# Kernel optimization log

Measured on AMD Instinct MI355X. Metric: run time of the kernel, lower is better.

The kernel has to match this reference:

```python
import jax, jax.numpy as jnp
import numpy as np

DIM = 512

def setup_inputs() -> dict:
    key = jax.random.key(0)
    ks = jax.random.split(key, 8)
    B, T, S, D = 4, 128, 512, DIM
    scale = 1.0 / np.sqrt(D)
    return {
        "inp": jax.random.normal(ks[0], (B, T, D), jnp.float32),
        "context": jax.random.normal(ks[1], (B, S, D), jnp.float32),
        # linear_query: Linear(D, D, bias=True)
        "Wq": jax.random.normal(ks[2], (D, D), jnp.float32) * scale,
        "bq": jax.random.normal(ks[3], (D,), jnp.float32) * scale,
        # linear_context: Linear(D, D, bias=False)
        "Wc": jax.random.normal(ks[4], (D, D), jnp.float32) * scale,
        # v: Linear(D, 1, bias=False)
        "v": jax.random.normal(ks[5], (D,), jnp.float32) * scale,
        # linear_out: Linear(2D, D, bias=True)
        "Wout": jax.random.normal(ks[6], (D, 2 * D), jnp.float32) * scale,
        "bout": jax.random.normal(ks[7], (D,), jnp.float32) * scale,
    }

def reference(inp, context, Wq, bq, Wc, v, Wout, bout):
    # inp: (B,T,D) target queries; context: (B,S,D) source states
    wq = jnp.einsum('btd,ed->bte', inp, Wq) + bq          # (B,T,D)
    uh = jnp.einsum('bsd,ed->bse', context, Wc)            # (B,S,D)
    # additive (Bahdanau) score: v^T tanh(Wq q_t + Wc h_s)
    wquh = jnp.tanh(wq[:, :, None, :] + uh[:, None, :, :])  # (B,T,S,D)
    align = jnp.einsum('btsd,d->bts', wquh, v)             # (B,T,S)
    align_vectors = jax.nn.softmax(align, axis=-1)          # softmax over src_len
    c = jnp.einsum('bts,bsd->btd', align_vectors, context)  # context vector
    concat_c = jnp.concatenate([c, inp], axis=-1)           # (B,T,2D)
    attn_h = jnp.einsum('btf,ef->bte', concat_c, Wout) + bout  # (B,T,D)
    return attn_h, align_vectors
```

## Files before the change

### kernel.cpp

```cpp
#include <hip/hip_runtime.h>
#include <hip/hip_bf16.h>
#include <math.h>


typedef __attribute__((ext_vector_type(8))) short short8;
typedef __attribute__((ext_vector_type(4))) float f32x4;
typedef unsigned short ushort_t;

static __device__ __forceinline__ unsigned short f2bf(float x) {
    union { __hip_bfloat16 h; unsigned short u; } c;
    c.h = __float2bfloat16(x);
    return c.u;
}
static __device__ __forceinline__ int bf2x(float lo, float hi) {
    return (int)(((unsigned)f2bf(hi) << 16) | (unsigned)f2bf(lo));
}

template<bool BF>
static __device__ __forceinline__ void load16(const void* base, size_t elemoff,
                                              int4& r0, int4& r1) {
    if (BF) {
        const int4* p = (const int4*)((const ushort_t*)base + elemoff);
        r0 = p[0]; r1 = p[1];
    } else {
        const float4* p = (const float4*)((const float*)base + elemoff);
        float4 a = p[0], b = p[1], c = p[2], d = p[3];
        r0.x = bf2x(a.x, a.y); r0.y = bf2x(a.z, a.w);
        r0.z = bf2x(b.x, b.y); r0.w = bf2x(b.z, b.w);
        r1.x = bf2x(c.x, c.y); r1.y = bf2x(c.z, c.w);
        r1.z = bf2x(d.x, d.y); r1.w = bf2x(d.z, d.w);
    }
}

template<bool A_BF, bool W_BF, int EPI>
static __device__ __forceinline__ void gemm_body(
    ushort_t* As, ushort_t* Ws,
    const void* A, const void* W, const float* bias, const float* partial,
    void* Cv, int K, int lda, int ldw, int ldc, int bm, int bn)
{
    const int tid = threadIdx.x;
    const int wave = tid >> 6, lane = tid & 63;
    const int mh = (wave & 1) * 32, nh = (wave >> 1) * 32;
    const int quad = lane >> 4, l16 = lane & 15;
    const int srow = tid >> 2, schunk = tid & 3;

    const size_t aoff = (size_t)(bm + srow) * lda + schunk * 16;
    const size_t woff = (size_t)(bn + srow) * ldw + schunk * 16;
    int4* AsW = (int4*)&As[srow * 72 + schunk * 16];
    int4* WsW = (int4*)&Ws[srow * 72 + schunk * 16];

    f32x4 acc00 = {0.f, 0.f, 0.f, 0.f}, acc01 = acc00, acc10 = acc00, acc11 = acc00;

    int4 a0r, a1r, w0r, w1r;
    load16<A_BF>(A, aoff, a0r, a1r);
    load16<W_BF>(W, woff, w0r, w1r);

    for (int k0 = 0; k0 < K; k0 += 64) {
        AsW[0] = a0r; AsW[1] = a1r;
        WsW[0] = w0r; WsW[1] = w1r;
        __syncthreads();
        if (k0 + 64 < K) {
            load16<A_BF>(A, aoff + k0 + 64, a0r, a1r);
            load16<W_BF>(W, woff + k0 + 64, w0r, w1r);
        }
        #pragma unroll
        for (int kk = 0; kk < 64; kk += 32) {
            short8 a0 = *(const short8*)&As[(mh + l16) * 72 + kk + quad * 8];
            short8 a1 = *(const short8*)&As[(mh + 16 + l16) * 72 + kk + quad * 8];
            short8 b0 = *(const short8*)&Ws[(nh + l16) * 72 + kk + quad * 8];
            short8 b1 = *(const short8*)&Ws[(nh + 16 + l16) * 72 + kk + quad * 8];
            acc00 = __builtin_amdgcn_mfma_f32_16x16x32_bf16(a0, b0, acc00, 0, 0, 0);
            acc01 = __builtin_amdgcn_mfma_f32_16x16x32_bf16(a0, b1, acc01, 0, 0, 0);
            acc10 = __builtin_amdgcn_mfma_f32_16x16x32_bf16(a1, b0, acc10, 0, 0, 0);
            acc11 = __builtin_amdgcn_mfma_f32_16x16x32_bf16(a1, b1, acc11, 0, 0, 0);
        }
        __syncthreads();
    }

    const int col0 = bn + nh + l16;
    const int col1 = col0 + 16;
    float bias0 = bias ? bias[col0] : 0.f;
    float bias1 = bias ? bias[col1] : 0.f;

    f32x4 accs[2][2] = {{acc00, acc01}, {acc10, acc11}};
    #pragma unroll
    for (int mt = 0; mt < 2; ++mt) {
        #pragma unroll
        for (int r = 0; r < 4; ++r) {
            int row = bm + mh + mt * 16 + quad * 4 + r;
            size_t rowoff = (size_t)row * ldc;
            float v0 = accs[mt][0][r] + bias0;
            float v1 = accs[mt][1][r] + bias1;
            if (EPI == 1) { v0 = __expf(2.f * v0); v1 = __expf(2.f * v1); }
            if (EPI == 3) { v0 += partial[rowoff + col0]; v1 += partial[rowoff + col1]; }
            if (EPI == 2) {
                ushort_t* C = (ushort_t*)Cv;
                C[rowoff + col0] = f2bf(v0);
                C[rowoff + col1] = f2bf(v1);
            } else {
                float* C = (float*)Cv;
                C[rowoff + col0] = v0;
                C[rowoff + col1] = v1;
            }
        }
    }
}

__global__ __launch_bounds__(256) void cvt_bf16(
    const float* __restrict__ inp, const float* __restrict__ ctx,
    const float* __restrict__ Wq, const float* __restrict__ Wc,
    const float* __restrict__ Wout,
    ushort_t* __restrict__ inpb, ushort_t* __restrict__ ctxb,
    ushort_t* __restrict__ Wqb, ushort_t* __restrict__ Wcb,
    ushort_t* __restrict__ Woutb)
{
    const int bid = blockIdx.x;
    const float* src; ushort_t* dst; int base;
    if (bid < 128)      { src = inp;  dst = inpb;  base = bid; }
    else if (bid < 640) { src = ctx;  dst = ctxb;  base = bid - 128; }
    else if (bid < 768) { src = Wq;   dst = Wqb;   base = bid - 640; }
    else if (bid < 896) { src = Wc;   dst = Wcb;   base = bid - 768; }
    else                { src = Wout; dst = Woutb; base = bid - 896; }
    const size_t off = (size_t)base * 2048 + (size_t)threadIdx.x * 8;
    const float4* s = (const float4*)(src + off);
    float4 a = s[0], b = s[1];
    int4 r;
    r.x = bf2x(a.x, a.y); r.y = bf2x(a.z, a.w);
    r.z = bf2x(b.x, b.y); r.w = bf2x(b.z, b.w);
    *(int4*)(dst + off) = r;
}

__global__ __launch_bounds__(256) void fused_front(
    const ushort_t* __restrict__ inpb, const ushort_t* __restrict__ ctxb,
    const ushort_t* __restrict__ Wqb, const float* __restrict__ bq,
    const ushort_t* __restrict__ Wcb, const ushort_t* __restrict__ Woutb,
    const float* __restrict__ bout,
    float* __restrict__ Ew, float* __restrict__ Eu, float* __restrict__ Y0,
    ushort_t* __restrict__ GT)
{
    __shared__ ushort_t As[64 * 72];
    __shared__ ushort_t Ws[64 * 72];
    const int bid = blockIdx.x;

    if (bid < 64) {
        gemm_body<true, true, 1>(As, Ws, inpb, Wqb, bq, nullptr, Ew,
                                 512, 512, 512, 512, (bid & 7) * 64, (bid >> 3) * 64);
    } else if (bid < 320) {
        int i = bid - 64;
        gemm_body<true, true, 1>(As, Ws, ctxb, Wcb, nullptr, nullptr, Eu,
                                 512, 512, 512, 512, (i & 31) * 64, (i >> 5) * 64);
    } else if (bid < 576) {
        int i = bid - 320;
        int b = i >> 6, j = i & 63;
        gemm_body<true, true, 2>(As, Ws, Woutb, ctxb + (size_t)b * 262144, nullptr,
                                 nullptr, GT + (size_t)b * 262144,
                                 512, 1024, 512, 512, (j & 7) * 64, (j >> 3) * 64);
    } else {
        int i = bid - 576;
        gemm_body<true, true, 0>(As, Ws, inpb, Woutb + 512, bout, nullptr, Y0,
                                 512, 512, 1024, 512, (i & 7) * 64, (i >> 3) * 64);
    }
}

__global__ __launch_bounds__(256) void align_kernel(
    const float* __restrict__ Ew, const float* __restrict__ Eu,
    const float* __restrict__ v, float* __restrict__ out)
{
    const int lane = threadIdx.x & 63, wave = threadIdx.x >> 6;
    const int b = blockIdx.z;
    const int t0 = blockIdx.y * 16 + wave * 4;
    const int s0 = blockIdx.x * 8;

    const float* wp = Ew + (((size_t)(b * 128 + t0)) << 9);
    const float* up = Eu + (((size_t)(b * 512 + s0)) << 9);

    float acc[4][8];
    #pragma unroll
    for (int i = 0; i < 4; ++i)
        #pragma unroll
        for (int j = 0; j < 8; ++j) acc[i][j] = 0.f;
    float vsum = 0.f;

    for (int k0 = 0; k0 < 512; k0 += 128) {
        float va = v[k0 + lane];
        float vb = v[k0 + 64 + lane];
        vsum += va + vb;
        float wa[4], wb[4];
        #pragma unroll
        for (int i = 0; i < 4; ++i) {
            wa[i] = wp[i * 512 + k0 + lane];
            wb[i] = wp[i * 512 + k0 + 64 + lane];
        }
        #pragma unroll
        for (int j = 0; j < 8; ++j) {
            const float* u = up + ((size_t)j << 9) + k0 + lane;
            float ua = u[0];
            float ub = u[64];
            #pragma unroll
            for (int i = 0; i < 4; ++i) {
                float A = fmaf(wa[i], ua, 1.f);
                float B = fmaf(wb[i], ub, 1.f);
                float num = fmaf(va, B, vb * A);
                float r = __builtin_amdgcn_rcpf(A * B);
                acc[i][j] = fmaf(num, r, acc[i][j]);
            }
        }
    }

    float V = vsum;
    #pragma unroll
    for (int off = 32; off; off >>= 1) V += __shfl_xor(V, off, 64);

    float r0 = 0.f, r1 = 0.f, r2 = 0.f, r3 = 0.f;
    #pragma unroll
    for (int j = 0; j < 8; ++j) {
        float a0 = acc[0][j], a1 = acc[1][j], a2 = acc[2][j], a3 = acc[3][j];
        #pragma unroll
        for (int off = 32; off; off >>= 1) {
            a0 += __shfl_xor(a0, off, 64);
            a1 += __shfl_xor(a1, off, 64);
            a2 += __shfl_xor(a2, off, 64);
            a3 += __shfl_xor(a3, off, 64);
        }
        if (lane == j) {
            r0 = fmaf(-2.f, a0, V);
            r1 = fmaf(-2.f, a1, V);
            r2 = fmaf(-2.f, a2, V);
            r3 = fmaf(-2.f, a3, V);
        }
    }
    if (lane < 8) {
        size_t o = (((size_t)(b * 128 + t0)) << 9) + s0 + lane;
        out[o] = r0;
        out[o + 512] = r1;
        out[o + 1024] = r2;
        out[o + 1536] = r3;
    }
}

__global__ __launch_bounds__(256) void softmax_512(
    const float* __restrict__ Sraw, float* __restrict__ alignv,
    ushort_t* __restrict__ pbf)
{
    const int row = blockIdx.x;
    const float* p = Sraw + ((size_t)row << 9);
    float* a = alignv + ((size_t)row << 9);
    ushort_t* q = pbf + ((size_t)row << 9);
    const int tid = threadIdx.x;
    float x0 = p[tid];
    float x1 = p[tid + 256];

    float m = fmaxf(x0, x1);
    #pragma unroll
    for (int off = 32; off > 0; off >>= 1)
        m = fmaxf(m, __shfl_xor(m, off, 64));
    __shared__ float redm[4];
    __shared__ float reds[4];
    const int wave = tid >> 6;
    if ((tid & 63) == 0) redm[wave] = m;
    __syncthreads();
    m = fmaxf(fmaxf(redm[0], redm[1]), fmaxf(redm[2], redm[3]));

    float e0 = __expf(x0 - m);
    float e1 = __expf(x1 - m);
    float s = e0 + e1;
    #pragma unroll
    for (int off = 32; off > 0; off >>= 1)
        s += __shfl_xor(s, off, 64);
    if ((tid & 63) == 0) reds[wave] = s;
    __syncthreads();
    s = reds[0] + reds[1] + reds[2] + reds[3];
    float r = 1.0f / s;
    float p0 = e0 * r, p1 = e1 * r;
    a[tid] = p0;
    a[tid + 256] = p1;
    q[tid] = f2bf(p0);
    q[tid + 256] = f2bf(p1);
}

__global__ __launch_bounds__(256) void gemm_att(
    const ushort_t* __restrict__ P, const ushort_t* __restrict__ GT,
    const float* __restrict__ Y0, float* __restrict__ attn)
{
    __shared__ ushort_t As[64 * 72];
    __shared__ ushort_t Ws[64 * 72];
    const int b = blockIdx.z;
    gemm_body<true, true, 3>(As, Ws,
                             P + (size_t)b * 65536, GT + (size_t)b * 262144,
                             nullptr, Y0 + (size_t)b * 65536,
                             attn + (size_t)b * 65536,
                             512, 512, 512, 512, blockIdx.x * 64, blockIdx.y * 64);
}

extern "C" void kernel_launch(void* const* d_in, const int* in_sizes, int n_in,
                              void* d_out, int out_size, void* d_ws, size_t ws_size,
                              hipStream_t stream)
{
    const float* inp  = (const float*)d_in[0];
    const float* ctx  = (const float*)d_in[1];
    const float* Wq   = (const float*)d_in[2];
    const float* bq   = (const float*)d_in[3];
    const float* Wc   = (const float*)d_in[4];
    const float* v    = (const float*)d_in[5];
    const float* Wout = (const float*)d_in[6];
    const float* bout = (const float*)d_in[7];

    float* out    = (float*)d_out;
    float* attn   = out;
    float* alignv = out + 262144;

    float* ws = (float*)d_ws;
    float* Ew   = ws;
    float* Eu   = ws + 262144;
    float* Y0   = ws + 1310720;
    float* Sraw = ws + 1572864;
    ushort_t* GT   = (ushort_t*)(ws + 1835008);
    ushort_t* P_bf = (ushort_t*)(ws + 2359296);
    ushort_t* inpb  = (ushort_t*)(ws + 2490368);
    ushort_t* ctxb  = (ushort_t*)(ws + 2621440);
    ushort_t* Wqb   = (ushort_t*)(ws + 3145728);
    ushort_t* Wcb   = (ushort_t*)(ws + 3276800);
    ushort_t* Woutb = (ushort_t*)(ws + 3407872);

    cvt_bf16<<<dim3(1152), 256, 0, stream>>>(inp, ctx, Wq, Wc, Wout,
                                             inpb, ctxb, Wqb, Wcb, Woutb);
    fused_front<<<dim3(640), 256, 0, stream>>>(inpb, ctxb, Wqb, bq, Wcb, Woutb,
                                               bout, Ew, Eu, Y0, GT);
    align_kernel<<<dim3(64, 8, 4), 256, 0, stream>>>(Ew, Eu, v, Sraw);
    softmax_512<<<dim3(512), 256, 0, stream>>>(Sraw, alignv, P_bf);
    gemm_att<<<dim3(2, 8, 4), 256, 0, stream>>>(P_bf, GT, Y0, attn);
}
```

Before: 116.6 us.

## Use recursive-halving shuffle reduction and drop max pass from softmax

Replaces the per-output butterfly reductions in align_kernel with a recursive-halving transpose-reduce, so all 32 outputs are reduced together with far fewer shuffles. The exponential is now computed in align_kernel, so the softmax kernel becomes a plain sum-and-normalize pass with no max reduction and one fewer barrier. Skipping the max subtraction assumes the scores are bounded, which holds here because the tanh-based score cannot exceed the sum of |v|. That bound is what keeps the unshifted exp from overflowing.

```diff
diff --git a/kernel.cpp b/kernel.cpp
--- a/kernel.cpp
+++ b/kernel.cpp
@@ -211,65 +211,86 @@
     #pragma unroll
     for (int off = 32; off; off >>= 1) V += __shfl_xor(V, off, 64);
 
-    float r0 = 0.f, r1 = 0.f, r2 = 0.f, r3 = 0.f;
-    #pragma unroll
-    for (int j = 0; j < 8; ++j) {
-        float a0 = acc[0][j], a1 = acc[1][j], a2 = acc[2][j], a3 = acc[3][j];
-        #pragma unroll
-        for (int off = 32; off; off >>= 1) {
-            a0 += __shfl_xor(a0, off, 64);
-            a1 += __shfl_xor(a1, off, 64);
-            a2 += __shfl_xor(a2, off, 64);
-            a3 += __shfl_xor(a3, off, 64);
-        }
-        if (lane == j) {
-            r0 = fmaf(-2.f, a0, V);
-            r1 = fmaf(-2.f, a1, V);
-            r2 = fmaf(-2.f, a2, V);
-            r3 = fmaf(-2.f, a3, V);
-        }
-    }
-    if (lane < 8) {
-        size_t o = (((size_t)(b * 128 + t0)) << 9) + s0 + lane;
-        out[o] = r0;
-        out[o + 512] = r1;
-        out[o + 1024] = r2;
-        out[o + 1536] = r3;
-    }
-}
-
-__global__ __launch_bounds__(256) void softmax_512(
-    const float* __restrict__ Sraw, float* __restrict__ alignv,
+    float x16[16];
+    {
+        const bool hb = lane & 1;
+        #pragma unroll
+        for (int i = 0; i < 4; ++i)
+            #pragma unroll
+            for (int m = 0; m < 4; ++m) {
+                float keep = hb ? acc[i][2 * m + 1] : acc[i][2 * m];
+                float send = hb ? acc[i][2 * m]     : acc[i][2 * m + 1];
+                x16[i * 4 + m] = keep + __shfl_xor(send, 1, 64);
+            }
+    }
+    float x8[8];
+    {
+        const bool hb = lane & 2;
+        #pragma unroll
+        for (int m = 0; m < 8; ++m) {
+            float keep = hb ? x16[2 * m + 1] : x16[2 * m];
+            float send = hb ? x16[2 * m]     : x16[2 * m + 1];
+            x8[m] = keep + __shfl_xor(send, 2, 64);
+        }
+    }
+    float x4[4];
+    {
+        const bool hb = lane & 4;
+        #pragma unroll
+        for (int m = 0; m < 4; ++m) {
+            float keep = hb ? x8[2 * m + 1] : x8[2 * m];
+            float send = hb ? x8[2 * m]     : x8[2 * m + 1];
+            x4[m] = keep + __shfl_xor(send, 4, 64);
+        }
+    }
+    float x2[2];
+    {
+        const bool hb = lane & 8;
+        #pragma unroll
+        for (int m = 0; m < 2; ++m) {
+            float keep = hb ? x4[2 * m + 1] : x4[2 * m];
+            float send = hb ? x4[2 * m]     : x4[2 * m + 1];
+            x2[m] = keep + __shfl_xor(send, 8, 64);
+        }
+    }
+    float x1;
+    {
+        const bool hb = lane & 16;
+        float keep = hb ? x2[1] : x2[0];
+        float send = hb ? x2[0] : x2[1];
+        x1 = keep + __shfl_xor(send, 16, 64);
+    }
+    x1 += __shfl_xor(x1, 32, 64);
+
+    const int oi = (lane >> 3) & 3;
+    const int oj = lane & 7;
+    float e = __expf(fmaf(-2.f, x1, V));
+    if (lane < 32) {
+        out[(((size_t)(b * 128 + t0 + oi)) << 9) + s0 + oj] = e;
+    }
+}
+
+__global__ __launch_bounds__(256) void normalize_512(
+    const float* __restrict__ E, float* __restrict__ alignv,
     ushort_t* __restrict__ pbf)
 {
     const int row = blockIdx.x;
-    const float* p = Sraw + ((size_t)row << 9);
+    const float* p = E + ((size_t)row << 9);
     float* a = alignv + ((size_t)row << 9);
     ushort_t* q = pbf + ((size_t)row << 9);
     const int tid = threadIdx.x;
-    float x0 = p[tid];
-    float x1 = p[tid + 256];
-
-    float m = fmaxf(x0, x1);
-    #pragma unroll
-    for (int off = 32; off > 0; off >>= 1)
-        m = fmaxf(m, __shfl_xor(m, off, 64));
-    __shared__ float redm[4];
-    __shared__ float reds[4];
-    const int wave = tid >> 6;
-    if ((tid & 63) == 0) redm[wave] = m;
-    __syncthreads();
-    m = fmaxf(fmaxf(redm[0], redm[1]), fmaxf(redm[2], redm[3]));
-
-    float e0 = __expf(x0 - m);
-    float e1 = __expf(x1 - m);
+    float e0 = p[tid];
+    float e1 = p[tid + 256];
+
     float s = e0 + e1;
     #pragma unroll
     for (int off = 32; off > 0; off >>= 1)
         s += __shfl_xor(s, off, 64);
+    __shared__ float reds[4];
+    const int wave = tid >> 6;
     if ((tid & 63) == 0) reds[wave] = s;
     __syncthreads();
-    s = reds[0] + reds[1] + reds[2] + reds[3];
+    s = (reds[0] + reds[1]) + (reds[2] + reds[3]);
     float r = 1.0f / s;
     float p0 = e0 * r, p1 = e1 * r;
     a[tid] = p0;
@@ -313,7 +334,7 @@
     float* Ew   = ws;
     float* Eu   = ws + 262144;
     float* Y0   = ws + 1310720;
-    float* Sraw = ws + 1572864;
+    float* E    = ws + 1572864;
     ushort_t* GT   = (ushort_t*)(ws + 1835008);
     ushort_t* P_bf = (ushort_t*)(ws + 2359296);
     ushort_t* inpb  = (ushort_t*)(ws + 2490368);
@@ -326,7 +347,7 @@
                                              inpb, ctxb, Wqb, Wcb, Woutb);
     fused_front<<<dim3(640), 256, 0, stream>>>(inpb, ctxb, Wqb, bq, Wcb, Woutb,
                                                bout, Ew, Eu, Y0, GT);
-    align_kernel<<<dim3(64, 8, 4), 256, 0, stream>>>(Ew, Eu, v, Sraw);
-    softmax_512<<<dim3(512), 256, 0, stream>>>(Sraw, alignv, P_bf);
+    align_kernel<<<dim3(64, 8, 4), 256, 0, stream>>>(Ew, Eu, v, E);
+    normalize_512<<<dim3(512), 256, 0, stream>>>(E, alignv, P_bf);
     gemm_att<<<dim3(2, 8, 4), 256, 0, stream>>>(P_bf, GT, Y0, attn);
 }
```

Result: faster. 110.3 us (-5.4%).
